# Optimization experiments

Measured on AMD Instinct MI355X. Metric: run time of the kernel, lower is better.

The kernel has to match this reference:

```python
import jax, jax.numpy as jnp
import numpy as np

N_POINTS = 65536
N0 = 65536
N_NEIGH = 32
K = 15
IN_F = 64
OUT_F = 128
RADIUS = 0.1
KP_EXTENT = 1.2 * RADIUS / 5.0  # config.KP_extent * radius / density_parameter
BN_EPS = 1e-6
NEG_SLOPE = 0.1


def setup_inputs() -> dict:
    key = jax.random.key(0)
    ks = jax.random.split(key, 8)
    cloud_scale = 0.05  # neighbor offsets ~ KP_EXTENT so influences are nonzero
    query_points = jax.random.uniform(ks[0], (N_POINTS, 3), jnp.float32) * cloud_scale
    support_points = jax.random.uniform(ks[1], (N0, 3), jnp.float32) * cloud_scale
    neighbors_indices = jax.random.randint(ks[2], (N_POINTS, N_NEIGH), 0, N0, jnp.int32)
    features = jax.random.normal(ks[3], (N0, IN_F), jnp.float32)
    # fixed kernel point dispositions, scaled to the kernel extent
    kernel_points = jax.random.normal(ks[4], (K, 3), jnp.float32) * (KP_EXTENT / 1.5)
    W = jax.random.normal(ks[5], (K, IN_F, OUT_F), jnp.float32) * np.sqrt(2.0 / OUT_F)
    gamma = jnp.ones((OUT_F,), jnp.float32)
    beta = jnp.zeros((OUT_F,), jnp.float32)
    return {
        "query_points": query_points,
        "support_points": support_points,
        "neighbors_indices": neighbors_indices,
        "features": features,
        "kernel_points": kernel_points,
        "W": W,
        "gamma": gamma,
        "beta": beta,
    }


def reference(query_points, support_points, neighbors_indices, features,
              kernel_points, W, gamma, beta):
    # --- KPConv: gather neighbors, kernel-point linear influence, sum aggregation ---
    # shadow point far away with zero features (handles out-of-range indices in original)
    sp = jnp.concatenate([support_points,
                          jnp.full((1, 3), 1e6, support_points.dtype)], axis=0)
    feat = jnp.concatenate([features,
                            jnp.zeros((1, features.shape[1]), features.dtype)], axis=0)
    neighbors = sp[neighbors_indices]                      # [n, m, 3]
    diffs = neighbors - query_points[:, None, :]           # [n, m, 3]
    # squared distances to each kernel point: [n, m, K]
    sq = jnp.sum((diffs[:, :, None, :] - kernel_points[None, None, :, :]) ** 2, axis=-1)
    # linear influence, 'sum' aggregation mode
    all_w = jnp.maximum(0.0, 1.0 - jnp.sqrt(sq) / KP_EXTENT)  # [n, m, K]
    all_w = jnp.transpose(all_w, (0, 2, 1))                   # [n, K, m]
    neighb_x = feat[neighbors_indices]                        # [n, m, in]
    weighted = jnp.einsum('nkm,nmi->nki', all_w, neighb_x)    # [n, K, in]
    x = jnp.einsum('nki,kio->no', weighted, W)                # [n, out]
    # --- BatchNorm1d (training-mode batch stats) + LeakyReLU(0.1) ---
    mean = jnp.mean(x, axis=0)
    var = jnp.var(x, axis=0)
    x = (x - mean) * jax.lax.rsqrt(var + BN_EPS) * gamma + beta
    return jnp.where(x >= 0, x, NEG_SLOPE * x)
```

## Files before the change

kernel.cpp:

```cpp
#include <hip/hip_runtime.h>

#define NPTS  65536
#define NNEI  32
#define NKP   15
#define INF   64
#define OUTF  128
#define PPB   16
#define KT_N  32
#define NSETS 64
#define INV_KPE 41.666666666666664f
#define BN_EPS 1e-6f
#define NEG_SLOPE 0.1f
#define INV_N (1.0f / 65536.0f)

typedef __attribute__((ext_vector_type(8))) short  bf16x8;
typedef __attribute__((ext_vector_type(4))) float  f32x4;

__device__ unsigned short g_Wp[KT_N * 8 * 64 * 8];
__device__ unsigned short g_featb[NPTS * INF];
__device__ __align__(16) unsigned short g_xb[NPTS * OUTF];
__device__ float g_part[NSETS][2 * OUTF];

__device__ __forceinline__ float b2f(unsigned short u) {
    union { unsigned int i; float f; } v; v.i = ((unsigned int)u) << 16; return v.f;
}
__device__ __forceinline__ unsigned short f2b(float f) {
    union { float f; unsigned int i; } v; v.f = f;
    unsigned int x = v.i;
    return (unsigned short)((x + 0x7fffu + ((x >> 16) & 1u)) >> 16);
}
__device__ __forceinline__ unsigned int pk2(float a, float b) {
    return (unsigned int)f2b(a) | ((unsigned int)f2b(b) << 16);
}
__device__ __forceinline__ bf16x8 mk8(unsigned int a, unsigned int b,
                                      unsigned int c, unsigned int d) {
    unsigned int t[4] = {a, b, c, d};
    bf16x8 r; __builtin_memcpy(&r, t, 16); return r;
}

__global__ __launch_bounds__(256) void pack_inputs(const float* __restrict__ W,
                                                   const float* __restrict__ feat) {
    const int b = blockIdx.x, t = threadIdx.x;
    if (b < NSETS) g_part[b][t] = 0.0f;
    if (b < 512) {
        int id = b * 256 + t;
        int j  = id & 7;
        int ln = (id >> 3) & 63;
        int nt = (id >> 9) & 7;
        int kt = id >> 12;
        int i  = kt * 32 + ((ln >> 4) * 8) + j;
        int kp = i & 15;
        int ch = i >> 4;
        int o  = nt * 16 + (ln & 15);
        g_Wp[id] = (kp < NKP) ? f2b(W[(kp * 64 + ch) * 128 + o]) : (unsigned short)0;
    } else {
        int id = (b - 512) * 256 + t;
        const float4 v = ((const float4*)feat)[id];
        uint2 r; r.x = pk2(v.x, v.y); r.y = pk2(v.z, v.w);
        ((uint2*)g_featb)[id] = r;
    }
}

__global__ __launch_bounds__(256, 4) void kpconv_fused(
        const float* __restrict__ qp,
        const float* __restrict__ sp,
        const int*   __restrict__ nbr,
        const float* __restrict__ kp)
{
    __shared__ __align__(16) unsigned short wlds[128 * PPB * 8];
    __shared__ float dbuf[4][128][3];
    __shared__ int   ibuf[4][128];

    const int tid  = threadIdx.x;
    const int lane = tid & 63;
    const int wv   = tid >> 6;
    const int q    = lane >> 4;
    const int c16  = lane & 15;
    const int gp0  = blockIdx.x * PPB + wv * 4;

#pragma unroll
    for (int rep = 0; rep < 2; ++rep) {
        const int pt  = rep * 2 + (lane >> 5);
        const int m   = lane & 31;
        const int gpt = gp0 + pt;
        const int idx = nbr[gpt * NNEI + m];
        ibuf[wv][pt * 32 + m] = idx;
        dbuf[wv][pt * 32 + m][0] = sp[idx * 3 + 0] - qp[gpt * 3 + 0];
        dbuf[wv][pt * 32 + m][1] = sp[idx * 3 + 1] - qp[gpt * 3 + 1];
        dbuf[wv][pt * 32 + m][2] = sp[idx * 3 + 2] - qp[gpt * 3 + 2];
    }
    float kx, ky, kz;
    if (c16 < NKP) { kx = kp[c16 * 3]; ky = kp[c16 * 3 + 1]; kz = kp[c16 * 3 + 2]; }
    else           { kx = ky = kz = 1.0e6f; }

    uint2 d[4][8];
#pragma unroll
    for (int pt = 0; pt < 4; ++pt) {
#pragma unroll
        for (int j = 0; j < 8; ++j) {
            const int idx = ibuf[wv][pt * 32 + q * 8 + j];
            d[pt][j] = *(const uint2*)&g_featb[idx * INF + c16 * 4];
        }
    }

#pragma unroll
    for (int pt = 0; pt < 4; ++pt) {
        const int pl = wv * 4 + pt;

        float w8[8];
#pragma unroll
        for (int j = 0; j < 8; ++j) {
            const int m = pt * 32 + q * 8 + j;
            const float ex = dbuf[wv][m][0] - kx;
            const float ey = dbuf[wv][m][1] - ky;
            const float ez = dbuf[wv][m][2] - kz;
            const float s  = ex * ex + ey * ey + ez * ez;
            const float w  = 1.0f - __builtin_amdgcn_sqrtf(s) * INV_KPE;
            w8[j] = (w > 0.0f) ? w : 0.0f;
        }
        const bf16x8 af = mk8(pk2(w8[0], w8[1]), pk2(w8[2], w8[3]),
                              pk2(w8[4], w8[5]), pk2(w8[6], w8[7]));

        f32x4 acc[4] = {{0.f,0.f,0.f,0.f},{0.f,0.f,0.f,0.f},
                        {0.f,0.f,0.f,0.f},{0.f,0.f,0.f,0.f}};
#pragma unroll
        for (int nt = 0; nt < 4; ++nt) {
            unsigned int dw[4];
#pragma unroll
            for (int p = 0; p < 4; ++p) {
                const unsigned int lo = (nt < 2) ? d[pt][2 * p].x     : d[pt][2 * p].y;
                const unsigned int hi = (nt < 2) ? d[pt][2 * p + 1].x : d[pt][2 * p + 1].y;
                dw[p] = (nt & 1) ? ((lo >> 16) | (hi & 0xffff0000u))
                                 : ((lo & 0xffffu) | (hi << 16));
            }
            acc[nt] = __builtin_amdgcn_mfma_f32_16x16x32_bf16(
                af, mk8(dw[0], dw[1], dw[2], dw[3]), acc[nt], 0, 0, 0);
        }

#pragma unroll
        for (int nt = 0; nt < 4; ++nt) {
            uint2 pv;
            pv.x = pk2(acc[nt][0], acc[nt][1]);
            pv.y = pk2(acc[nt][2], acc[nt][3]);
            const int ibase = (c16 * 4 + nt) * 16 + q * 4;
            const int g   = ibase >> 3;
            const int off = ibase & 7;
            const int plx = pl ^ ((g >> 3) & 7);
            *(uint2*)&wlds[(g * PPB + plx) * 8 + off] = pv;
        }
    }
    __syncthreads();

    const int nt0 = wv * 2;
    f32x4 a00 = {0.f,0.f,0.f,0.f}, a01 = {0.f,0.f,0.f,0.f};

    for (int kt = 0; kt < KT_N; ++kt) {
        const int g   = kt * 4 + q;
        const int plx = c16 ^ ((g >> 3) & 7);
        const bf16x8 fa  = *(const bf16x8*)&wlds[(g * PPB + plx) * 8];
        const bf16x8 fb0 = *(const bf16x8*)&g_Wp[((kt * 8 + nt0) * 64 + lane) * 8];
        const bf16x8 fb1 = *(const bf16x8*)&g_Wp[((kt * 8 + nt0 + 1) * 64 + lane) * 8];
        a00 = __builtin_amdgcn_mfma_f32_16x16x32_bf16(fa, fb0, a00, 0, 0, 0);
        a01 = __builtin_amdgcn_mfma_f32_16x16x32_bf16(fa, fb1, a01, 0, 0, 0);
    }

    const int rb = blockIdx.x * PPB + q * 4;
    const int c0 = nt0 * 16 + c16;
    float s0 = 0.f, q0 = 0.f, s1 = 0.f, q1 = 0.f;
#pragma unroll
    for (int r = 0; r < 4; ++r) {
        const float v0 = a00[r], v1 = a01[r];
        g_xb[(rb + r) * OUTF + c0]      = f2b(v0);
        g_xb[(rb + r) * OUTF + c0 + 16] = f2b(v1);
        s0 += v0; q0 += v0 * v0;
        s1 += v1; q1 += v1 * v1;
    }
    s0 += __shfl_xor(s0, 16); s0 += __shfl_xor(s0, 32);
    q0 += __shfl_xor(q0, 16); q0 += __shfl_xor(q0, 32);
    s1 += __shfl_xor(s1, 16); s1 += __shfl_xor(s1, 32);
    q1 += __shfl_xor(q1, 16); q1 += __shfl_xor(q1, 32);
    const int set = blockIdx.x & (NSETS - 1);
    if (lane < 16) {
        atomicAdd(&g_part[set][nt0 * 16 + lane],             s0);
        atomicAdd(&g_part[set][OUTF + nt0 * 16 + lane],      q0);
        atomicAdd(&g_part[set][nt0 * 16 + 16 + lane],        s1);
        atomicAdd(&g_part[set][OUTF + nt0 * 16 + 16 + lane], q1);
    }
}

__global__ __launch_bounds__(256) void bn_norm(const float* __restrict__ gamma,
                                               const float* __restrict__ beta,
                                               float* __restrict__ out) {
    __shared__ float ssc[OUTF], ssf[OUTF];
    const int t = threadIdx.x;
    if (t < OUTF) {
        float s = 0.f, qq = 0.f;
#pragma unroll 8
        for (int i = 0; i < NSETS; ++i) { s += g_part[i][t]; qq += g_part[i][OUTF + t]; }
        const float mean = s * INV_N;
        const float var  = qq * INV_N - mean * mean;
        const float sc   = gamma[t] * rsqrtf(var + BN_EPS);
        ssc[t] = sc;
        ssf[t] = beta[t] - mean * sc;
    }
    __syncthreads();

#pragma unroll
    for (int it = 0; it < 4; ++it) {
        const int id   = (blockIdx.x * 4 + it) * 256 + t;
        const int base = id * 8;
        const int o0   = base & 127;
        const uint4 v  = *(const uint4*)&g_xb[base];
        const unsigned int wds[4] = {v.x, v.y, v.z, v.w};
        float y[8];
#pragma unroll
        for (int p = 0; p < 4; ++p) {
            const float x0 = b2f((unsigned short)(wds[p] & 0xffffu));
            const float x1 = b2f((unsigned short)(wds[p] >> 16));
            float y0 = x0 * ssc[o0 + 2 * p]     + ssf[o0 + 2 * p];
            float y1 = x1 * ssc[o0 + 2 * p + 1] + ssf[o0 + 2 * p + 1];
            y[2 * p]     = (y0 >= 0.f) ? y0 : NEG_SLOPE * y0;
            y[2 * p + 1] = (y1 >= 0.f) ? y1 : NEG_SLOPE * y1;
        }
        float4 r0 = {y[0], y[1], y[2], y[3]};
        float4 r1 = {y[4], y[5], y[6], y[7]};
        *(float4*)&out[base]     = r0;
        *(float4*)&out[base + 4] = r1;
    }
}

extern "C" void kernel_launch(void* const* d_in, const int* in_sizes, int n_in,
                              void* d_out, int out_size, void* d_ws, size_t ws_size,
                              hipStream_t stream) {
    const float* qp    = (const float*)d_in[0];
    const float* sp    = (const float*)d_in[1];
    const int*   nbr   = (const int*)d_in[2];
    const float* feat  = (const float*)d_in[3];
    const float* kp    = (const float*)d_in[4];
    const float* W     = (const float*)d_in[5];
    const float* gamma = (const float*)d_in[6];
    const float* beta  = (const float*)d_in[7];
    float* out = (float*)d_out;

    pack_inputs<<<512 + 4096, 256, 0, stream>>>(W, feat);
    kpconv_fused<<<NPTS / PPB, 256, 0, stream>>>(qp, sp, nbr, kp);
    bn_norm<<<1024, 256, 0, stream>>>(gamma, beta, out);
}
```

Measured before the change: 190.4 us.

## Split bf16 feature table into channel halves and software-pipeline neighbor gathers

The bf16 feature table is repacked into two tables, each holding 32 channels per row. The main kernel now gathers neighbor features one point at a time in two channel phases, prefetching the next point's gather while it runs MFMAs on the current one. The kernel-point weights are computed once in the first phase and reused in the second. This cuts the live gather registers from 64 to about 16 and overlaps load latency with compute. In exchange it issues twice as many, narrower gather loads, touches two separate rows per neighbor, and keeps fewer loads in flight at once.

```diff
diff --git a/kernel.cpp b/kernel.cpp
--- a/kernel.cpp
+++ b/kernel.cpp
@@ -17,7 +17,8 @@
 typedef __attribute__((ext_vector_type(4))) float  f32x4;
 
 __device__ unsigned short g_Wp[KT_N * 8 * 64 * 8];
-__device__ unsigned short g_featb[NPTS * INF];
+__device__ unsigned short g_fb0[NPTS * 32];
+__device__ unsigned short g_fb1[NPTS * 32];
 __device__ __align__(16) unsigned short g_xb[NPTS * OUTF];
 __device__ float g_part[NSETS][2 * OUTF];
 
@@ -54,10 +55,13 @@
         int o  = nt * 16 + (ln & 15);
         g_Wp[id] = (kp < NKP) ? f2b(W[(kp * 64 + ch) * 128 + o]) : (unsigned short)0;
     } else {
-        int id = (b - 512) * 256 + t;
+        int id  = (b - 512) * 256 + t;
+        int row = id >> 4;
+        int c4  = (id & 15) * 4;
         const float4 v = ((const float4*)feat)[id];
         uint2 r; r.x = pk2(v.x, v.y); r.y = pk2(v.z, v.w);
-        ((uint2*)g_featb)[id] = r;
+        unsigned short* dst = (c4 < 32) ? g_fb0 : g_fb1;
+        *(uint2*)&dst[row * 32 + (c4 & 31)] = r;
     }
 }
 
@@ -93,60 +97,76 @@
     if (c16 < NKP) { kx = kp[c16 * 3]; ky = kp[c16 * 3 + 1]; kz = kp[c16 * 3 + 2]; }
     else           { kx = ky = kz = 1.0e6f; }
 
-    uint2 d[4][8];
-#pragma unroll
-    for (int pt = 0; pt < 4; ++pt) {
+    bf16x8 af[4];
+
+#pragma unroll
+    for (int ph = 0; ph < 2; ++ph) {
+        const unsigned short* tab = ph ? g_fb1 : g_fb0;
+
+        unsigned int dcur[8], dnxt[8];
 #pragma unroll
         for (int j = 0; j < 8; ++j) {
-            const int idx = ibuf[wv][pt * 32 + q * 8 + j];
-            d[pt][j] = *(const uint2*)&g_featb[idx * INF + c16 * 4];
+            const int idx = ibuf[wv][q * 8 + j];
+            dcur[j] = *(const unsigned int*)&tab[idx * 32 + c16 * 2];
         }
-    }
-
-#pragma unroll
-    for (int pt = 0; pt < 4; ++pt) {
-        const int pl = wv * 4 + pt;
-
-        float w8[8];
-#pragma unroll
-        for (int j = 0; j < 8; ++j) {
-            const int m = pt * 32 + q * 8 + j;
-            const float ex = dbuf[wv][m][0] - kx;
-            const float ey = dbuf[wv][m][1] - ky;
-            const float ez = dbuf[wv][m][2] - kz;
-            const float s  = ex * ex + ey * ey + ez * ez;
-            const float w  = 1.0f - __builtin_amdgcn_sqrtf(s) * INV_KPE;
-            w8[j] = (w > 0.0f) ? w : 0.0f;
-        }
-        const bf16x8 af = mk8(pk2(w8[0], w8[1]), pk2(w8[2], w8[3]),
-                              pk2(w8[4], w8[5]), pk2(w8[6], w8[7]));
-
-        f32x4 acc[4] = {{0.f,0.f,0.f,0.f},{0.f,0.f,0.f,0.f},
-                        {0.f,0.f,0.f,0.f},{0.f,0.f,0.f,0.f}};
-#pragma unroll
-        for (int nt = 0; nt < 4; ++nt) {
-            unsigned int dw[4];
+
+#pragma unroll
+        for (int pt = 0; pt < 4; ++pt) {
+            const int pl = wv * 4 + pt;
+
+            if (pt < 3) {
+#pragma unroll
+                for (int j = 0; j < 8; ++j) {
+                    const int idx = ibuf[wv][(pt + 1) * 32 + q * 8 + j];
+                    dnxt[j] = *(const unsigned int*)&tab[idx * 32 + c16 * 2];
+                }
+            }
+
+            if (ph == 0) {
+                float w8[8];
+#pragma unroll
+                for (int j = 0; j < 8; ++j) {
+                    const int m = pt * 32 + q * 8 + j;
+                    const float ex = dbuf[wv][m][0] - kx;
+                    const float ey = dbuf[wv][m][1] - ky;
+                    const float ez = dbuf[wv][m][2] - kz;
+                    const float s  = ex * ex + ey * ey + ez * ez;
+                    const float w  = 1.0f - __builtin_amdgcn_sqrtf(s) * INV_KPE;
+                    w8[j] = (w > 0.0f) ? w : 0.0f;
+                }
+                af[pt] = mk8(pk2(w8[0], w8[1]), pk2(w8[2], w8[3]),
+                             pk2(w8[4], w8[5]), pk2(w8[6], w8[7]));
+            }
+
+            unsigned int dw0[4], dw1[4];
 #pragma unroll
             for (int p = 0; p < 4; ++p) {
-                const unsigned int lo = (nt < 2) ? d[pt][2 * p].x     : d[pt][2 * p].y;
-                const unsigned int hi = (nt < 2) ? d[pt][2 * p + 1].x : d[pt][2 * p + 1].y;
-                dw[p] = (nt & 1) ? ((lo >> 16) | (hi & 0xffff0000u))
-                                 : ((lo & 0xffffu) | (hi << 16));
-            }
-            acc[nt] = __builtin_amdgcn_mfma_f32_16x16x32_bf16(
-                af, mk8(dw[0], dw[1], dw[2], dw[3]), acc[nt], 0, 0, 0);
-        }
-
-#pragma unroll
-        for (int nt = 0; nt < 4; ++nt) {
-            uint2 pv;
-            pv.x = pk2(acc[nt][0], acc[nt][1]);
-            pv.y = pk2(acc[nt][2], acc[nt][3]);
-            const int ibase = (c16 * 4 + nt) * 16 + q * 4;
-            const int g   = ibase >> 3;
-            const int off = ibase & 7;
-            const int plx = pl ^ ((g >> 3) & 7);
-            *(uint2*)&wlds[(g * PPB + plx) * 8 + off] = pv;
+                const unsigned int lo = dcur[2 * p];
+                const unsigned int hi = dcur[2 * p + 1];
+                dw0[p] = (lo & 0xffffu) | (hi << 16);
+                dw1[p] = (lo >> 16) | (hi & 0xffff0000u);
+            }
+            f32x4 acc0 = {0.f, 0.f, 0.f, 0.f}, acc1 = {0.f, 0.f, 0.f, 0.f};
+            acc0 = __builtin_amdgcn_mfma_f32_16x16x32_bf16(
+                af[pt], mk8(dw0[0], dw0[1], dw0[2], dw0[3]), acc0, 0, 0, 0);
+            acc1 = __builtin_amdgcn_mfma_f32_16x16x32_bf16(
+                af[pt], mk8(dw1[0], dw1[1], dw1[2], dw1[3]), acc1, 0, 0, 0);
+
+#pragma unroll
+            for (int nt = 0; nt < 2; ++nt) {
+                const f32x4 a = nt ? acc1 : acc0;
+                uint2 pv;
+                pv.x = pk2(a[0], a[1]);
+                pv.y = pk2(a[2], a[3]);
+                const int ibase = (ph * 32 + c16 * 2 + nt) * 16 + q * 4;
+                const int g   = ibase >> 3;
+                const int off = ibase & 7;
+                const int plx = pl ^ ((g >> 3) & 7);
+                *(uint2*)&wlds[(g * PPB + plx) * 8 + off] = pv;
+            }
+
+#pragma unroll
+            for (int j = 0; j < 8; ++j) dcur[j] = dnxt[j];
         }
     }
     __syncthreads();
```

Measured after the change: 203.1 us. 1.07x slower.
